# Kernel optimization log

Measured on AMD Instinct MI355X. Metric: run time of the kernel, lower is better.

Reference implementation:

```python
import jax, jax.numpy as jnp
import numpy as np

B = 32; H = 56; W = 56; C = 192; WS = 7; SHIFT = 3; NH = 6
HD = C // NH; N = WS * WS; MLP = 4 * C; NWH = H // WS; NWW = W // WS
EPS = 1e-5


def _rel_pos_index():
    coords = np.stack(np.meshgrid(np.arange(WS), np.arange(WS), indexing='ij'))  # (2,WS,WS)
    cf = coords.reshape(2, -1)                      # (2, N)
    rel = (cf[:, :, None] - cf[:, None, :]).transpose(1, 2, 0).astype(np.int64)  # (N,N,2)
    rel[..., 0] += WS - 1
    rel[..., 1] += WS - 1
    rel[..., 0] *= 2 * WS - 1
    return jnp.asarray(rel.sum(-1))                 # (N, N) int

REL_IDX = _rel_pos_index()


def _shift_mask():
    img = np.zeros((1, H, W, 1), np.float32)
    cnt = 0
    for hs in (slice(0, -WS), slice(-WS, -SHIFT), slice(-SHIFT, None)):
        for ws_ in (slice(0, -WS), slice(-WS, -SHIFT), slice(-SHIFT, None)):
            img[:, hs, ws_, :] = cnt
            cnt += 1
    mw = img.reshape(1, NWH, WS, NWW, WS, 1).transpose(0, 1, 3, 2, 4, 5).reshape(-1, N)
    am = mw[:, None, :] - mw[:, :, None]
    return jnp.asarray(np.where(am != 0, -100.0, 0.0).astype(np.float32))  # (nW, N, N)


def setup_inputs() -> dict:
    key = jax.random.key(0)
    ks = jax.random.split(key, 8)
    s = 0.02
    return {
        'x': jax.random.normal(ks[0], (B, H * W, C), jnp.float32),
        'attn_mask': _shift_mask(),
        'norm1_w': jnp.ones((C,), jnp.float32),
        'norm1_b': jnp.zeros((C,), jnp.float32),
        'qkv_w': jax.random.normal(ks[1], (3 * C, C), jnp.float32) * s,
        'qkv_b': jnp.zeros((3 * C,), jnp.float32),
        'rpb_table': jax.random.normal(ks[2], ((2 * WS - 1) ** 2, NH), jnp.float32) * s,
        'proj_w': jax.random.normal(ks[3], (C, C), jnp.float32) * s,
        'proj_b': jnp.zeros((C,), jnp.float32),
        'norm2_w': jnp.ones((C,), jnp.float32),
        'norm2_b': jnp.zeros((C,), jnp.float32),
        'fc1_w': jax.random.normal(ks[4], (MLP, C), jnp.float32) * s,
        'fc1_b': jnp.zeros((MLP,), jnp.float32),
        'fc2_w': jax.random.normal(ks[5], (C, MLP), jnp.float32) * s,
        'fc2_b': jnp.zeros((C,), jnp.float32),
    }


def _ln(x, w, b):
    m = jnp.mean(x, axis=-1, keepdims=True)
    v = jnp.mean(jnp.square(x - m), axis=-1, keepdims=True)
    return (x - m) * jax.lax.rsqrt(v + EPS) * w + b


def reference(x, attn_mask, norm1_w, norm1_b, qkv_w, qkv_b, rpb_table,
              proj_w, proj_b, norm2_w, norm2_b, fc1_w, fc1_b, fc2_w, fc2_b):
    shortcut = x
    xs = _ln(x, norm1_w, norm1_b).reshape(B, H, W, C)
    # cyclic shift
    xs = jnp.roll(xs, (-SHIFT, -SHIFT), axis=(1, 2))
    # window partition -> (B*nW, N, C)
    xw = xs.reshape(B, NWH, WS, NWW, WS, C).transpose(0, 1, 3, 2, 4, 5).reshape(-1, N, C)
    B_ = xw.shape[0]
    # qkv
    qkv = xw @ qkv_w.T + qkv_b                       # (B_, N, 3C)
    qkv = qkv.reshape(B_, N, 3, NH, HD).transpose(2, 0, 3, 1, 4)
    q, k, v = qkv[0], qkv[1], qkv[2]                 # (B_, NH, N, HD)
    scale = HD ** -0.5
    attn = jnp.einsum('bhnd,bhmd->bhnm', q * scale, k)
    # relative position bias: (N,N,NH) -> (NH,N,N)
    bias = rpb_table[REL_IDX.reshape(-1)].reshape(N, N, NH).transpose(2, 0, 1)
    attn = attn + bias[None]
    # shift mask: (nW, N, N)
    nW = attn_mask.shape[0]
    attn = attn.reshape(B_ // nW, nW, NH, N, N) + attn_mask[None, :, None]
    attn = jax.nn.softmax(attn.reshape(B_, NH, N, N), axis=-1)
    out = jnp.einsum('bhnm,bhmd->bhnd', attn, v)     # (B_, NH, N, HD)
    out = out.transpose(0, 2, 1, 3).reshape(B_, N, C)
    out = out @ proj_w.T + proj_b
    # window reverse -> (B, H, W, C)
    xr = out.reshape(B, NWH, NWW, WS, WS, C).transpose(0, 1, 3, 2, 4, 5).reshape(B, H, W, C)
    xr = jnp.roll(xr, (SHIFT, SHIFT), axis=(1, 2)).reshape(B, H * W, C)
    x = shortcut + xr
    # MLP
    h = _ln(x, norm2_w, norm2_b)
    h = jax.nn.gelu(h @ fc1_w.T + fc1_b, approximate=False)
    h = h @ fc2_w.T + fc2_b
    return x + h
```

## Files before the change

### kernel.cpp

```cpp
#include <hip/hip_runtime.h>
#include <hip/hip_bf16.h>

typedef unsigned short u16;
typedef __attribute__((ext_vector_type(8))) short bf16x8;
typedef __attribute__((ext_vector_type(4))) float f32x4;

#define MFMA16(a, b, c) __builtin_amdgcn_mfma_f32_16x16x32_bf16(a, b, c, 0, 0, 0)

__device__ __forceinline__ u16 f2b(float f) {
  union { float f; unsigned u; } x; x.f = f;
  return (u16)((x.u + 0x7fffu + ((x.u >> 16) & 1u)) >> 16);
}

__device__ __forceinline__ void gload_lds16(const void* g, void* l) {
  __builtin_amdgcn_global_load_lds(
      (const __attribute__((address_space(1))) void*)g,
      (__attribute__((address_space(3))) void*)l, 16, 0, 0);
}

template <int NCH>
__device__ __forceinline__ void stage_frags(const u16* __restrict__ src,
                                            u16* dst, int wave, int lane) {
#pragma unroll
  for (int it = 0; it < NCH / 4; ++it) {
    int chunk = it * 4 + wave;
    gload_lds16(src + ((size_t)chunk * 64 + lane) * 8, dst + chunk * 512);
  }
}

__device__ __forceinline__ void stage_64x192(const u16* __restrict__ src,
                                             int stride, u16* dst, int wave,
                                             int lane) {
#pragma unroll
  for (int it = 0; it < 6; ++it) {
    int id = (it * 4 + wave) * 64 + lane;
    int row = id / 24, ph = id - row * 24;
    int lch = (ph & 24) | ((ph ^ (row & 7)) & 7);
    gload_lds16(src + (size_t)row * stride + lch * 8,
                dst + (it * 4 + wave) * 512);
  }
}

__global__ __launch_bounds__(256) void pack_kernel(const float* __restrict__ W,
                                                   u16* __restrict__ F, int NT,
                                                   int KS, int K, int kmajor) {
  int f = blockIdx.x * 256 + threadIdx.x;
  if (f >= NT * KS * 64) return;
  int l = f & 63, rest = f >> 6;
  int ks, ct;
  if (kmajor) { ct = rest % NT; ks = rest / NT; }
  else        { ks = rest % KS; ct = rest / KS; }
  int row = ct * 16 + (l & 15);
  int col = ks * 32 + (l >> 4) * 8;
  const float* s = W + (size_t)row * K + col;
  u16* d = F + (size_t)f * 8;
#pragma unroll
  for (int i = 0; i < 8; ++i) d[i] = f2b(s[i]);
}

__global__ __launch_bounds__(256) void pack2_kernel(const float* __restrict__ W,
                                                    u16* __restrict__ F) {
  int f = blockIdx.x * 256 + threadIdx.x;
  if (f >= 24 * 12 * 64) return;
  int l = f & 63, rest = f >> 6;
  int ct = rest % 12, hs = rest / 12;
  int row = ct * 16 + (l & 15);
  int g = l >> 4;
  u16* d = F + (size_t)f * 8;
#pragma unroll
  for (int i = 0; i < 8; ++i) {
    int h = hs * 32 + (i < 4 ? 4 * g + i : 16 + 4 * g + (i - 4));
    d[i] = f2b(W[(size_t)row * 768 + h]);
  }
}

__global__ __launch_bounds__(256, 3) void attn_win(
    const float* __restrict__ x, const float* __restrict__ n1w,
    const float* __restrict__ n1b, const u16* __restrict__ qkvwf,
    const float* __restrict__ qkvb_, const float* __restrict__ rpb,
    const float* __restrict__ amask, u16* __restrict__ aout, int win0) {
  __shared__ __align__(16) u16 lds[25088];
  u16* wbuf = lds;
  u16* sA   = lds;
  u16* klds = lds + 18432;
  u16* vlds = lds + 21000;
  int tid = threadIdx.x, wave = tid >> 6, lane = tid & 63;
  int g = lane >> 4, c = lane & 15, wr = wave * 16;
  int blk = blockIdx.x;
  int wing = win0 + blk;
  int wi = wing & 63;
  {
    float vals[12][4];
    int srcrow[4];
#pragma unroll
    for (int reg = 0; reg < 4; ++reg) {
      int n = wr + 4 * g + reg;
      if (n > 48) n = 48;
      int bb = wing >> 6, wloc = wing & 63, wh = wloc >> 3, ww = wloc & 7;
      int rr = n / 7, cc = n - rr * 7;
      int hs = wh * 7 + rr + 3; if (hs >= 56) hs -= 56;
      int wsr = ww * 7 + cc + 3; if (wsr >= 56) wsr -= 56;
      srcrow[reg] = bb * 3136 + hs * 56 + wsr;
    }
#pragma unroll
    for (int nt = 0; nt < 12; ++nt)
#pragma unroll
      for (int reg = 0; reg < 4; ++reg)
        vals[nt][reg] = x[(size_t)srcrow[reg] * 192 + nt * 16 + c];
#pragma unroll
    for (int reg = 0; reg < 4; ++reg) {
      float s = 0.f;
#pragma unroll
      for (int nt = 0; nt < 12; ++nt) s += vals[nt][reg];
      s += __shfl_xor(s, 1, 64); s += __shfl_xor(s, 2, 64);
      s += __shfl_xor(s, 4, 64); s += __shfl_xor(s, 8, 64);
      float m = s * (1.f / 192.f), q = 0.f;
#pragma unroll
      for (int nt = 0; nt < 12; ++nt) { float d = vals[nt][reg] - m; q += d * d; }
      q += __shfl_xor(q, 1, 64); q += __shfl_xor(q, 2, 64);
      q += __shfl_xor(q, 4, 64); q += __shfl_xor(q, 8, 64);
      float rs = rsqrtf(q * (1.f / 192.f) + 1e-5f);
#pragma unroll
      for (int nt = 0; nt < 12; ++nt) vals[nt][reg] = (vals[nt][reg] - m) * rs;
    }
#pragma unroll
    for (int nt = 0; nt < 12; ++nt) {
      float wv = n1w[nt * 16 + c], bv = n1b[nt * 16 + c];
#pragma unroll
      for (int reg = 0; reg < 4; ++reg) {
        int r = wr + 4 * g + reg;
        int ch = nt * 2 + (c >> 3);
        int ph = (ch & 24) | ((ch ^ (r & 7)) & 7);
        sA[r * 192 + ph * 8 + (c & 7)] = f2b(vals[nt][reg] * wv + bv);
      }
    }
  }
  __syncthreads();
  bf16x8 afr[6];
  {
    int ar = wr + c;
#pragma unroll
    for (int ks = 0; ks < 6; ++ks) {
      int ch = ks * 4 + g;
      int ph = (ch & 24) | ((ch ^ (ar & 7)) & 7);
      afr[ks] = *(const bf16x8*)(sA + ar * 192 + ph * 8);
    }
  }
  __syncthreads();
#pragma unroll
  for (int s = 0; s < 3; ++s)
    stage_frags<12>(qkvwf + (size_t)((s * 12 + 0) * 6) * 512, wbuf + s * 6144,
                    wave, lane);
  int nq = wr + c;
  int nb = nq > 48 ? 48 : nq;
  int ridx[16];
  float pm[16];
  {
    int i1 = nb / 7, j1 = nb - i1 * 7;
#pragma unroll
    for (int kt = 0; kt < 4; ++kt)
#pragma unroll
      for (int reg = 0; reg < 4; ++reg) {
        int m = kt * 16 + 4 * g + reg;
        int idx = kt * 4 + reg;
        if (m < 49) {
          int i2 = m / 7, j2 = m - i2 * 7;
          ridx[idx] = ((i1 - i2 + 6) * 13 + (j1 - j2 + 6)) * 6;
          pm[idx] = amask[(size_t)wi * 2401 + nb * 49 + m];
        } else {
          ridx[idx] = 0;
          pm[idx] = -1e30f;
        }
      }
  }
  __syncthreads();
  for (int h = 0; h < 6; ++h) {
    f32x4 qa[2], ka[2], va[2];
#pragma unroll
    for (int s = 0; s < 3; ++s)
#pragma unroll
      for (int t = 0; t < 2; ++t) {
        f32x4 acc = {0.f, 0.f, 0.f, 0.f};
#pragma unroll
        for (int ks = 0; ks < 6; ++ks) {
          bf16x8 wf = *(const bf16x8*)(wbuf + (s * 12 + t * 6 + ks) * 512 +
                                       lane * 8);
          acc = MFMA16(wf, afr[ks], acc);
        }
        float4 b4 = *(const float4*)(qkvb_ + s * 192 + h * 32 + t * 16 + 4 * g);
#pragma unroll
        for (int reg = 0; reg < 4; ++reg) acc[reg] += ((const float*)&b4)[reg];
        if (s == 0) qa[t] = acc;
        else if (s == 1) ka[t] = acc;
        else va[t] = acc;
      }
    union { u16 hh[8]; bf16x8 v; } qf, kf;
#pragma unroll
    for (int reg = 0; reg < 4; ++reg) {
      qf.hh[reg] = f2b(qa[0][reg]);
      qf.hh[reg + 4] = f2b(qa[1][reg]);
      kf.hh[reg] = f2b(ka[0][reg]);
      kf.hh[reg + 4] = f2b(ka[1][reg]);
    }
    *(bf16x8*)(klds + nq * 40 + g * 8) = kf.v;
#pragma unroll
    for (int t = 0; t < 2; ++t)
#pragma unroll
      for (int reg = 0; reg < 4; ++reg)
        vlds[(t * 16 + 4 * g + reg) * 68 + nq] = f2b(va[t][reg]);
    __syncthreads();
    if (h < 5) {
#pragma unroll
      for (int s = 0; s < 3; ++s)
        stage_frags<12>(qkvwf + (size_t)((s * 12 + (h + 1) * 2) * 6) * 512,
                        wbuf + s * 6144, wave, lane);
    }
    float sv[16];
#pragma unroll
    for (int kt = 0; kt < 4; ++kt) {
      bf16x8 kw = *(const bf16x8*)(klds + (kt * 16 + c) * 40 + g * 8);
      f32x4 z = {0.f, 0.f, 0.f, 0.f};
      f32x4 sacc = MFMA16(kw, qf.v, z);
#pragma unroll
      for (int reg = 0; reg < 4; ++reg) sv[kt * 4 + reg] = sacc[reg];
    }
    const float scale = 0.17677669529663687f;
    float mx = -1e30f;
#pragma unroll
    for (int i = 0; i < 16; ++i) {
      sv[i] = sv[i] * scale + rpb[ridx[i] + h] + pm[i];
      mx = fmaxf(mx, sv[i]);
    }
    mx = fmaxf(mx, __shfl_xor(mx, 16, 64));
    mx = fmaxf(mx, __shfl_xor(mx, 32, 64));
    float se = 0.f;
#pragma unroll
    for (int i = 0; i < 16; ++i) {
      sv[i] = __expf(sv[i] - mx);
      se += sv[i];
    }
    se += __shfl_xor(se, 16, 64);
    se += __shfl_xor(se, 32, 64);
    float inv = 1.0f / se;
    union { u16 hh[8]; bf16x8 v; } pu0, pu1;
#pragma unroll
    for (int reg = 0; reg < 4; ++reg) {
      pu0.hh[reg] = f2b(sv[0 * 4 + reg] * inv);
      pu0.hh[reg + 4] = f2b(sv[1 * 4 + reg] * inv);
      pu1.hh[reg] = f2b(sv[2 * 4 + reg] * inv);
      pu1.hh[reg + 4] = f2b(sv[3 * 4 + reg] * inv);
    }
    f32x4 oacc[2] = {{0, 0, 0, 0}, {0, 0, 0, 0}};
#pragma unroll
    for (int nt = 0; nt < 2; ++nt)
#pragma unroll
      for (int mblk = 0; mblk < 2; ++mblk) {
        const u16* vp = vlds + (nt * 16 + c) * 68 + mblk * 32 + 4 * g;
        union { u16 hh[8]; bf16x8 v; } vt;
        *(short4*)(vt.hh) = *(const short4*)(vp);
        *(short4*)(vt.hh + 4) = *(const short4*)(vp + 16);
        oacc[nt] = MFMA16(vt.v, mblk ? pu1.v : pu0.v, oacc[nt]);
      }
    if (nq < 49) {
      u16* op = aout + ((size_t)blk * 49 + nq) * 192 + h * 32;
#pragma unroll
      for (int nt = 0; nt < 2; ++nt) {
        ushort4 st;
        st.x = f2b(oacc[nt][0]);
        st.y = f2b(oacc[nt][1]);
        st.z = f2b(oacc[nt][2]);
        st.w = f2b(oacc[nt][3]);
        *(ushort4*)(op + nt * 16 + 4 * g) = st;
      }
    }
    __syncthreads();
  }
}

__global__ __launch_bounds__(256, 3) void proj_fused(
    const u16* __restrict__ aout, const u16* __restrict__ wf,
    const float* __restrict__ pb, const float* __restrict__ x,
    float* __restrict__ out, int tok0) {
  __shared__ __align__(16) u16 lds[24576];
  u16* sA = lds;
  u16* b0 = lds;
  u16* b1 = lds + 12288;
  int tid = threadIdx.x, wave = tid >> 6, lane = tid & 63;
  int g = lane >> 4, c = lane & 15;
  int m0 = blockIdx.x * 64;
  stage_64x192(aout + (size_t)m0 * 192, 192, sA, wave, lane);
  asm volatile("s_waitcnt vmcnt(0)" ::: "memory");
  __syncthreads();
  int mw = wave >> 1, nw = wave & 1;
  bf16x8 afr[2][6];
#pragma unroll
  for (int rt = 0; rt < 2; ++rt) {
    int ar = mw * 32 + rt * 16 + c;
#pragma unroll
    for (int ks = 0; ks < 6; ++ks) {
      int ch = ks * 4 + g;
      int ph = (ch & 24) | ((ch ^ (ar & 7)) & 7);
      afr[rt][ks] = *(const bf16x8*)(sA + ar * 192 + ph * 8);
    }
  }
  size_t trow[2][4];
#pragma unroll
  for (int rt = 0; rt < 2; ++rt)
#pragma unroll
    for (int reg = 0; reg < 4; ++reg) {
      int rg = tok0 + m0 + mw * 32 + rt * 16 + 4 * g + reg;
      int win = rg / 49, n = rg - win * 49;
      int b_ = win >> 6, wi = win & 63;
      int wh = wi >> 3, ww = wi & 7;
      int rr = n / 7, cc = n - rr * 7;
      int hd_ = wh * 7 + rr + 3; if (hd_ >= 56) hd_ -= 56;
      int wd = ww * 7 + cc + 3; if (wd >= 56) wd -= 56;
      trow[rt][reg] = (size_t)b_ * 3136 + hd_ * 56 + wd;
    }
  __syncthreads();
  stage_frags<24>(wf, b0, wave, lane);
  __syncthreads();
  for (int j = 0; j < 3; ++j) {
    const u16* cb = (j & 1) ? b1 : b0;
    if (j < 2)
      stage_frags<24>(wf + (size_t)(j + 1) * 24 * 512, (j & 1) ? b0 : b1, wave,
                      lane);
    f32x4 S[2][2] = {{{0,0,0,0},{0,0,0,0}},{{0,0,0,0},{0,0,0,0}}};
#pragma unroll
    for (int nt = 0; nt < 2; ++nt)
#pragma unroll
      for (int ks = 0; ks < 6; ++ks) {
        bf16x8 bf = *(const bf16x8*)(cb + ((nw * 2 + nt) * 6 + ks) * 512 + lane * 8);
        S[0][nt] = MFMA16(afr[0][ks], bf, S[0][nt]);
        S[1][nt] = MFMA16(afr[1][ks], bf, S[1][nt]);
      }
#pragma unroll
    for (int nt = 0; nt < 2; ++nt) {
      int jc = j * 64 + nw * 32 + nt * 16 + c;
      float bv = pb[jc];
#pragma unroll
      for (int rt = 0; rt < 2; ++rt)
#pragma unroll
        for (int reg = 0; reg < 4; ++reg) {
          size_t o = trow[rt][reg] * 192 + jc;
          out[o] = x[o] + S[rt][nt][reg] + bv;
        }
    }
    __syncthreads();
  }
}

__global__ __launch_bounds__(256, 3) void mlp_fused(
    const float* __restrict__ n2w, const float* __restrict__ n2b,
    const u16* __restrict__ w1f, const float* __restrict__ b1,
    const u16* __restrict__ w2f, const float* __restrict__ b2,
    float* __restrict__ out) {
  __shared__ __align__(16) u16 lds[24576];
  u16* c1a = lds;
  u16* c1b = lds + 6144;
  u16* c2a = lds + 12288;
  u16* c2b = lds + 18432;
  u16* sA  = lds;
  int tid = threadIdx.x, wave = tid >> 6, lane = tid & 63;
  int g = lane >> 4, c = lane & 15, wr = wave * 16;
  int m0 = blockIdx.x * 64;
  {
    float v[12][4];
    int rr[4];
#pragma unroll
    for (int reg = 0; reg < 4; ++reg) rr[reg] = m0 + wr + 4 * g + reg;
#pragma unroll
    for (int nt = 0; nt < 12; ++nt)
#pragma unroll
      for (int reg = 0; reg < 4; ++reg)
        v[nt][reg] = out[(size_t)rr[reg] * 192 + nt * 16 + c];
#pragma unroll
    for (int reg = 0; reg < 4; ++reg) {
      float s = 0.f;
#pragma unroll
      for (int nt = 0; nt < 12; ++nt) s += v[nt][reg];
      s += __shfl_xor(s, 1, 64); s += __shfl_xor(s, 2, 64);
      s += __shfl_xor(s, 4, 64); s += __shfl_xor(s, 8, 64);
      float m = s * (1.f / 192.f), q = 0.f;
#pragma unroll
      for (int nt = 0; nt < 12; ++nt) { float d = v[nt][reg] - m; q += d * d; }
      q += __shfl_xor(q, 1, 64); q += __shfl_xor(q, 2, 64);
      q += __shfl_xor(q, 4, 64); q += __shfl_xor(q, 8, 64);
      float rs = rsqrtf(q * (1.f / 192.f) + 1e-5f);
#pragma unroll
      for (int nt = 0; nt < 12; ++nt) v[nt][reg] = (v[nt][reg] - m) * rs;
    }
#pragma unroll
    for (int nt = 0; nt < 12; ++nt) {
      float wv = n2w[nt * 16 + c], bv = n2b[nt * 16 + c];
#pragma unroll
      for (int reg = 0; reg < 4; ++reg) {
        int r = wr + 4 * g + reg;
        int ch = nt * 2 + (c >> 3);
        int ph = (ch & 24) | ((ch ^ (r & 7)) & 7);
        sA[r * 192 + ph * 8 + (c & 7)] = f2b(v[nt][reg] * wv + bv);
      }
    }
  }
  __syncthreads();
  bf16x8 afr[6];
  {
    int ar = wr + c;
#pragma unroll
    for (int ks = 0; ks < 6; ++ks) {
      int ch = ks * 4 + g;
      int ph = (ch & 24) | ((ch ^ (ar & 7)) & 7);
      afr[ks] = *(const bf16x8*)(sA + ar * 192 + ph * 8);
    }
  }
  __syncthreads();
  stage_frags<12>(w1f, c1a, wave, lane);
  stage_frags<12>(w2f, c2a, wave, lane);
  f32x4 o[12];
#pragma unroll
  for (int i = 0; i < 12; ++i) o[i] = (f32x4){0.f, 0.f, 0.f, 0.f};
  __syncthreads();
  for (int j = 0; j < 24; ++j) {
    int cur = j & 1;
    const u16* r1 = cur ? c1b : c1a;
    const u16* r2 = cur ? c2b : c2a;
    if (j < 23) {
      stage_frags<12>(w1f + (size_t)(j + 1) * 6144, cur ? c1a : c1b, wave, lane);
      stage_frags<12>(w2f + (size_t)(j + 1) * 6144, cur ? c2a : c2b, wave, lane);
    }
    f32x4 S1[2] = {{0,0,0,0},{0,0,0,0}};
#pragma unroll
    for (int ks = 0; ks < 6; ++ks) {
      bf16x8 w0 = *(const bf16x8*)(r1 + (0 * 6 + ks) * 512 + lane * 8);
      bf16x8 w1v = *(const bf16x8*)(r1 + (1 * 6 + ks) * 512 + lane * 8);
      S1[0] = MFMA16(w0, afr[ks], S1[0]);
      S1[1] = MFMA16(w1v, afr[ks], S1[1]);
    }
    union { u16 h[8]; bf16x8 v; } pu;
    float4 bv0 = *(const float4*)(b1 + j * 32 + 4 * g);
    float4 bv1 = *(const float4*)(b1 + j * 32 + 16 + 4 * g);
#pragma unroll
    for (int r = 0; r < 4; ++r) {
      float v0 = S1[0][r] + ((const float*)&bv0)[r];
      float u20 = v0 * (1.5957691216f + 0.0713548163f * v0 * v0);
      pu.h[r] = f2b(v0 / (1.f + __expf(-u20)));
      float v1 = S1[1][r] + ((const float*)&bv1)[r];
      float u21 = v1 * (1.5957691216f + 0.0713548163f * v1 * v1);
      pu.h[r + 4] = f2b(v1 / (1.f + __expf(-u21)));
    }
#pragma unroll
    for (int ct = 0; ct < 12; ++ct) {
      bf16x8 wf2 = *(const bf16x8*)(r2 + ct * 512 + lane * 8);
      o[ct] = MFMA16(wf2, pu.v, o[ct]);
    }
    __syncthreads();
  }
  size_t rowoff = (size_t)(m0 + wr + c) * 192;
#pragma unroll
  for (int ct = 0; ct < 12; ++ct) {
    float4 b4 = *(const float4*)(b2 + ct * 16 + 4 * g);
#pragma unroll
    for (int r = 0; r < 4; ++r) {
      size_t oo = rowoff + ct * 16 + 4 * g + r;
      out[oo] = out[oo] + o[ct][r] + ((const float*)&b4)[r];
    }
  }
}

extern "C" void kernel_launch(void* const* d_in, const int* in_sizes, int n_in,
                              void* d_out, int out_size, void* d_ws, size_t ws_size,
                              hipStream_t stream) {
  (void)in_sizes; (void)n_in; (void)out_size;
  const float* x     = (const float*)d_in[0];
  const float* amask = (const float*)d_in[1];
  const float* n1w   = (const float*)d_in[2];
  const float* n1b   = (const float*)d_in[3];
  const float* qkvw  = (const float*)d_in[4];
  const float* qkvb  = (const float*)d_in[5];
  const float* rpb   = (const float*)d_in[6];
  const float* projw = (const float*)d_in[7];
  const float* projb = (const float*)d_in[8];
  const float* n2w   = (const float*)d_in[9];
  const float* n2b   = (const float*)d_in[10];
  const float* fc1w  = (const float*)d_in[11];
  const float* fc1b  = (const float*)d_in[12];
  const float* fc2w  = (const float*)d_in[13];
  const float* fc2b  = (const float*)d_in[14];
  float* out = (float*)d_out;
  char* ws = (char*)d_ws;

  u16* qkvwf = (u16*)(ws);
  u16* projwf = (u16*)(ws + 221184);
  u16* fc1wf = (u16*)(ws + 221184 + 73728);
  u16* fc2wf = (u16*)(ws + 221184 + 73728 + 294912);
  char* arena = ws + (1 << 20);
  size_t arena_sz = ws_size > (1 << 20) ? ws_size - (1 << 20) : 0;

  pack_kernel<<<(36 * 6 * 64 + 255) / 256, 256, 0, stream>>>(qkvw, qkvwf, 36, 6, 192, 0);
  pack_kernel<<<(12 * 6 * 64 + 255) / 256, 256, 0, stream>>>(projw, projwf, 12, 6, 192, 0);
  pack_kernel<<<(48 * 6 * 64 + 255) / 256, 256, 0, stream>>>(fc1w, fc1wf, 48, 6, 192, 0);
  pack2_kernel<<<(24 * 12 * 64 + 255) / 256, 256, 0, stream>>>(fc2w, fc2wf);

  int NCA = 1;
  while (NCA < 16 && (size_t)(2048 / NCA) * 49 * 192 * 2 > arena_sz) NCA <<= 1;
  int Wc = 2048 / NCA;
  for (int cch = 0; cch < NCA; ++cch) {
    int win0 = cch * Wc;
    int tok0 = win0 * 49;
    u16* aout_c = (u16*)arena;
    int rows = Wc * 49;
    attn_win<<<Wc, 256, 0, stream>>>(x, n1w, n1b, qkvwf, qkvb, rpb, amask,
                                     aout_c, win0);
    proj_fused<<<rows / 64, 256, 0, stream>>>(aout_c, projwf, projb, x, out,
                                              tok0);
  }

  mlp_fused<<<1568, 256, 0, stream>>>(n2w, n2b, fc1wf, fc1b, fc2wf, fc2b,
                                      out);
}
```

Baseline: 265.9 us.

## Enlarge MLP block to 128 rows with 8 waves sharing staged weights

The fused MLP kernel now runs 512 threads per block and covers 128 rows instead of 64. Each double-buffered fc1/fc2 weight fragment staged into LDS is therefore reused by twice as many rows, which cuts weight load traffic and staging work per row. Staging is spread over 8 waves with a new helper, and the residual epilogue now uses float4 read-modify-write instead of scalar accesses. In exchange, LDS use and register pressure per block rise, and the grid drops to 784 blocks, which changes wave-quantization and occupancy.

```diff
diff --git a/kernel.cpp b/kernel.cpp
--- a/kernel.cpp
+++ b/kernel.cpp
@@ -25,6 +25,21 @@
   for (int it = 0; it < NCH / 4; ++it) {
     int chunk = it * 4 + wave;
     gload_lds16(src + ((size_t)chunk * 64 + lane) * 8, dst + chunk * 512);
+  }
+}
+
+__device__ __forceinline__ void stage12x2_512(const u16* __restrict__ s1,
+                                              u16* d1,
+                                              const u16* __restrict__ s2,
+                                              u16* d2, int wave, int lane) {
+#pragma unroll
+  for (int it = 0; it < 3; ++it) {
+    int id = it * 8 + wave;
+    if (id < 12)
+      gload_lds16(s1 + ((size_t)id * 64 + lane) * 8, d1 + id * 512);
+    else
+      gload_lds16(s2 + ((size_t)(id - 12) * 64 + lane) * 8,
+                  d2 + (id - 12) * 512);
   }
 }
 
@@ -350,7 +365,7 @@
   }
 }
 
-__global__ __launch_bounds__(256, 3) void mlp_fused(
+__global__ __launch_bounds__(512, 2) void mlp_fused(
     const float* __restrict__ n2w, const float* __restrict__ n2b,
     const u16* __restrict__ w1f, const float* __restrict__ b1,
     const u16* __restrict__ w2f, const float* __restrict__ b2,
@@ -363,7 +378,7 @@
   u16* sA  = lds;
   int tid = threadIdx.x, wave = tid >> 6, lane = tid & 63;
   int g = lane >> 4, c = lane & 15, wr = wave * 16;
-  int m0 = blockIdx.x * 64;
+  int m0 = blockIdx.x * 128;
   {
     float v[12][4];
     int rr[4];
@@ -414,8 +429,7 @@
     }
   }
   __syncthreads();
-  stage_frags<12>(w1f, c1a, wave, lane);
-  stage_frags<12>(w2f, c2a, wave, lane);
+  stage12x2_512(w1f, c1a, w2f, c2a, wave, lane);
   f32x4 o[12];
 #pragma unroll
   for (int i = 0; i < 12; ++i) o[i] = (f32x4){0.f, 0.f, 0.f, 0.f};
@@ -424,10 +438,9 @@
     int cur = j & 1;
     const u16* r1 = cur ? c1b : c1a;
     const u16* r2 = cur ? c2b : c2a;
-    if (j < 23) {
-      stage_frags<12>(w1f + (size_t)(j + 1) * 6144, cur ? c1a : c1b, wave, lane);
-      stage_frags<12>(w2f + (size_t)(j + 1) * 6144, cur ? c2a : c2b, wave, lane);
-    }
+    if (j < 23)
+      stage12x2_512(w1f + (size_t)(j + 1) * 6144, cur ? c1a : c1b,
+                    w2f + (size_t)(j + 1) * 6144, cur ? c2a : c2b, wave, lane);
     f32x4 S1[2] = {{0,0,0,0},{0,0,0,0}};
 #pragma unroll
     for (int ks = 0; ks < 6; ++ks) {
@@ -455,15 +468,17 @@
     }
     __syncthreads();
   }
-  size_t rowoff = (size_t)(m0 + wr + c) * 192;
+  float* rowp = out + (size_t)(m0 + wr + c) * 192;
 #pragma unroll
   for (int ct = 0; ct < 12; ++ct) {
+    float4* p = (float4*)(rowp + ct * 16 + 4 * g);
+    float4 cu = *p;
     float4 b4 = *(const float4*)(b2 + ct * 16 + 4 * g);
-#pragma unroll
-    for (int r = 0; r < 4; ++r) {
-      size_t oo = rowoff + ct * 16 + 4 * g + r;
-      out[oo] = out[oo] + o[ct][r] + ((const float*)&b4)[r];
-    }
+    cu.x += o[ct][0] + b4.x;
+    cu.y += o[ct][1] + b4.y;
+    cu.z += o[ct][2] + b4.z;
+    cu.w += o[ct][3] + b4.w;
+    *p = cu;
   }
 }
 
@@ -515,6 +530,6 @@
                                               tok0);
   }
 
-  mlp_fused<<<1568, 256, 0, stream>>>(n2w, n2b, fc1wf, fc1b, fc2wf, fc2b,
-                                      out);
-}
+  mlp_fused<<<784, 512, 0, stream>>>(n2w, n2b, fc1wf, fc1b, fc2wf, fc2b,
+                                     out);
+}
```

New measurement: 285.2 us. 1.07x slower.

## Fuse output projection and residual into attention window kernel

Applied to the files above, without the earlier changes.

The separate proj kernel and its bf16 attention-output buffer are removed. Each attention block keeps per-head outputs in registers as MFMA B-fragments, then stages a repacked projection weight (two halves) into LDS and computes proj plus bias plus residual directly, writing to the un-shifted token rows. This removes a global write and read of the attention output and a kernel launch, at the cost of more registers and per-block weight staging in attn_win.

```diff
diff --git a/kernel.cpp b/kernel.cpp
--- a/kernel.cpp
+++ b/kernel.cpp
@@ -25,19 +25,6 @@
   for (int it = 0; it < NCH / 4; ++it) {
     int chunk = it * 4 + wave;
     gload_lds16(src + ((size_t)chunk * 64 + lane) * 8, dst + chunk * 512);
-  }
-}
-
-__device__ __forceinline__ void stage_64x192(const u16* __restrict__ src,
-                                             int stride, u16* dst, int wave,
-                                             int lane) {
-#pragma unroll
-  for (int it = 0; it < 6; ++it) {
-    int id = (it * 4 + wave) * 64 + lane;
-    int row = id / 24, ph = id - row * 24;
-    int lch = (ph & 24) | ((ph ^ (row & 7)) & 7);
-    gload_lds16(src + (size_t)row * stride + lch * 8,
-                dst + (it * 4 + wave) * 512);
   }
 }
 
@@ -74,11 +61,29 @@
   }
 }
 
+__global__ __launch_bounds__(256) void pack_proj_pi(const float* __restrict__ W,
+                                                    u16* __restrict__ F) {
+  int f = blockIdx.x * 256 + threadIdx.x;
+  if (f >= 72 * 64) return;
+  int l = f & 63, rest = f >> 6;
+  int half = rest / 36, r2 = rest - half * 36;
+  int ks = r2 / 6, ctl = r2 - ks * 6;
+  int row = (half * 6 + ctl) * 16 + (l & 15);
+  int g = l >> 4;
+  u16* d = F + (size_t)f * 8;
+#pragma unroll
+  for (int i = 0; i < 8; ++i) {
+    int k = ks * 32 + (i < 4 ? 4 * g + i : 16 + 4 * g + (i - 4));
+    d[i] = f2b(W[(size_t)row * 192 + k]);
+  }
+}
+
 __global__ __launch_bounds__(256, 3) void attn_win(
     const float* __restrict__ x, const float* __restrict__ n1w,
     const float* __restrict__ n1b, const u16* __restrict__ qkvwf,
     const float* __restrict__ qkvb_, const float* __restrict__ rpb,
-    const float* __restrict__ amask, u16* __restrict__ aout, int win0) {
+    const float* __restrict__ amask, const u16* __restrict__ pwf,
+    const float* __restrict__ pb, float* __restrict__ out) {
   __shared__ __align__(16) u16 lds[25088];
   u16* wbuf = lds;
   u16* sA   = lds;
@@ -86,8 +91,7 @@
   u16* vlds = lds + 21000;
   int tid = threadIdx.x, wave = tid >> 6, lane = tid & 63;
   int g = lane >> 4, c = lane & 15, wr = wave * 16;
-  int blk = blockIdx.x;
-  int wing = win0 + blk;
+  int wing = blockIdx.x;
   int wi = wing & 63;
   {
     float vals[12][4];
@@ -174,6 +178,8 @@
       }
   }
   __syncthreads();
+  bf16x8 ofr[6];
+#pragma unroll
   for (int h = 0; h < 6; ++h) {
     f32x4 qa[2], ka[2], va[2];
 #pragma unroll
@@ -261,90 +267,60 @@
         *(short4*)(vt.hh + 4) = *(const short4*)(vp + 16);
         oacc[nt] = MFMA16(vt.v, mblk ? pu1.v : pu0.v, oacc[nt]);
       }
+    {
+      union { u16 hh[8]; bf16x8 v; } of_;
+#pragma unroll
+      for (int reg = 0; reg < 4; ++reg) {
+        of_.hh[reg] = f2b(oacc[0][reg]);
+        of_.hh[reg + 4] = f2b(oacc[1][reg]);
+      }
+      ofr[h] = of_.v;
+    }
+    __syncthreads();
+  }
+  size_t trow = 0;
+  if (nq < 49) {
+    int rr = nq / 7, cc2 = nq - rr * 7;
+    int wloc = wing & 63, wh = wloc >> 3, ww2 = wloc & 7;
+    int hs2 = wh * 7 + rr + 3; if (hs2 >= 56) hs2 -= 56;
+    int ws2 = ww2 * 7 + cc2 + 3; if (ws2 >= 56) ws2 -= 56;
+    trow = (size_t)(wing >> 6) * 3136 + hs2 * 56 + ws2;
+  }
+#pragma unroll
+  for (int half = 0; half < 2; ++half) {
+#pragma unroll
+    for (int it = 0; it < 9; ++it) {
+      int chunk = it * 4 + wave;
+      gload_lds16(pwf + ((size_t)(half * 36 + chunk) * 64 + lane) * 8,
+                  lds + chunk * 512);
+    }
+    asm volatile("s_waitcnt vmcnt(0)" ::: "memory");
+    __syncthreads();
+    f32x4 op6[6];
+#pragma unroll
+    for (int i = 0; i < 6; ++i) op6[i] = (f32x4){0.f, 0.f, 0.f, 0.f};
+#pragma unroll
+    for (int ks = 0; ks < 6; ++ks)
+#pragma unroll
+      for (int ctl = 0; ctl < 6; ++ctl) {
+        bf16x8 wf = *(const bf16x8*)(lds + (ks * 6 + ctl) * 512 + lane * 8);
+        op6[ctl] = MFMA16(wf, ofr[ks], op6[ctl]);
+      }
     if (nq < 49) {
-      u16* op = aout + ((size_t)blk * 49 + nq) * 192 + h * 32;
-#pragma unroll
-      for (int nt = 0; nt < 2; ++nt) {
-        ushort4 st;
-        st.x = f2b(oacc[nt][0]);
-        st.y = f2b(oacc[nt][1]);
-        st.z = f2b(oacc[nt][2]);
-        st.w = f2b(oacc[nt][3]);
-        *(ushort4*)(op + nt * 16 + 4 * g) = st;
-      }
-    }
-    __syncthreads();
-  }
-}
-
-__global__ __launch_bounds__(256, 3) void proj_fused(
-    const u16* __restrict__ aout, const u16* __restrict__ wf,
-    const float* __restrict__ pb, const float* __restrict__ x,
-    float* __restrict__ out, int tok0) {
-  __shared__ __align__(16) u16 lds[24576];
-  u16* sA = lds;
-  u16* b0 = lds;
-  u16* b1 = lds + 12288;
-  int tid = threadIdx.x, wave = tid >> 6, lane = tid & 63;
-  int g = lane >> 4, c = lane & 15;
-  int m0 = blockIdx.x * 64;
-  stage_64x192(aout + (size_t)m0 * 192, 192, sA, wave, lane);
-  asm volatile("s_waitcnt vmcnt(0)" ::: "memory");
-  __syncthreads();
-  int mw = wave >> 1, nw = wave & 1;
-  bf16x8 afr[2][6];
-#pragma unroll
-  for (int rt = 0; rt < 2; ++rt) {
-    int ar = mw * 32 + rt * 16 + c;
-#pragma unroll
-    for (int ks = 0; ks < 6; ++ks) {
-      int ch = ks * 4 + g;
-      int ph = (ch & 24) | ((ch ^ (ar & 7)) & 7);
-      afr[rt][ks] = *(const bf16x8*)(sA + ar * 192 + ph * 8);
-    }
-  }
-  size_t trow[2][4];
-#pragma unroll
-  for (int rt = 0; rt < 2; ++rt)
-#pragma unroll
-    for (int reg = 0; reg < 4; ++reg) {
-      int rg = tok0 + m0 + mw * 32 + rt * 16 + 4 * g + reg;
-      int win = rg / 49, n = rg - win * 49;
-      int b_ = win >> 6, wi = win & 63;
-      int wh = wi >> 3, ww = wi & 7;
-      int rr = n / 7, cc = n - rr * 7;
-      int hd_ = wh * 7 + rr + 3; if (hd_ >= 56) hd_ -= 56;
-      int wd = ww * 7 + cc + 3; if (wd >= 56) wd -= 56;
-      trow[rt][reg] = (size_t)b_ * 3136 + hd_ * 56 + wd;
-    }
-  __syncthreads();
-  stage_frags<24>(wf, b0, wave, lane);
-  __syncthreads();
-  for (int j = 0; j < 3; ++j) {
-    const u16* cb = (j & 1) ? b1 : b0;
-    if (j < 2)
-      stage_frags<24>(wf + (size_t)(j + 1) * 24 * 512, (j & 1) ? b0 : b1, wave,
-                      lane);
-    f32x4 S[2][2] = {{{0,0,0,0},{0,0,0,0}},{{0,0,0,0},{0,0,0,0}}};
-#pragma unroll
-    for (int nt = 0; nt < 2; ++nt)
-#pragma unroll
-      for (int ks = 0; ks < 6; ++ks) {
-        bf16x8 bf = *(const bf16x8*)(cb + ((nw * 2 + nt) * 6 + ks) * 512 + lane * 8);
-        S[0][nt] = MFMA16(afr[0][ks], bf, S[0][nt]);
-        S[1][nt] = MFMA16(afr[1][ks], bf, S[1][nt]);
-      }
-#pragma unroll
-    for (int nt = 0; nt < 2; ++nt) {
-      int jc = j * 64 + nw * 32 + nt * 16 + c;
-      float bv = pb[jc];
-#pragma unroll
-      for (int rt = 0; rt < 2; ++rt)
-#pragma unroll
-        for (int reg = 0; reg < 4; ++reg) {
-          size_t o = trow[rt][reg] * 192 + jc;
-          out[o] = x[o] + S[rt][nt][reg] + bv;
-        }
+      float* rowp = out + trow * 192 + half * 96;
+      const float* xp = x + trow * 192 + half * 96;
+#pragma unroll
+      for (int ctl = 0; ctl < 6; ++ctl) {
+        int colo = ctl * 16 + 4 * g;
+        float4 xv = *(const float4*)(xp + colo);
+        float4 b4 = *(const float4*)(pb + half * 96 + colo);
+        float4 st;
+        st.x = xv.x + op6[ctl][0] + b4.x;
+        st.y = xv.y + op6[ctl][1] + b4.y;
+        st.z = xv.z + op6[ctl][2] + b4.z;
+        st.w = xv.w + op6[ctl][3] + b4.w;
+        *(float4*)(rowp + colo) = st;
+      }
     }
     __syncthreads();
   }
@@ -470,7 +446,7 @@
 extern "C" void kernel_launch(void* const* d_in, const int* in_sizes, int n_in,
                               void* d_out, int out_size, void* d_ws, size_t ws_size,
                               hipStream_t stream) {
-  (void)in_sizes; (void)n_in; (void)out_size;
+  (void)in_sizes; (void)n_in; (void)out_size; (void)ws_size;
   const float* x     = (const float*)d_in[0];
   const float* amask = (const float*)d_in[1];
   const float* n1w   = (const float*)d_in[2];
@@ -493,27 +469,14 @@
   u16* projwf = (u16*)(ws + 221184);
   u16* fc1wf = (u16*)(ws + 221184 + 73728);
   u16* fc2wf = (u16*)(ws + 221184 + 73728 + 294912);
-  char* arena = ws + (1 << 20);
-  size_t arena_sz = ws_size > (1 << 20) ? ws_size - (1 << 20) : 0;
 
   pack_kernel<<<(36 * 6 * 64 + 255) / 256, 256, 0, stream>>>(qkvw, qkvwf, 36, 6, 192, 0);
-  pack_kernel<<<(12 * 6 * 64 + 255) / 256, 256, 0, stream>>>(projw, projwf, 12, 6, 192, 0);
+  pack_proj_pi<<<(72 * 64 + 255) / 256, 256, 0, stream>>>(projw, projwf);
   pack_kernel<<<(48 * 6 * 64 + 255) / 256, 256, 0, stream>>>(fc1w, fc1wf, 48, 6, 192, 0);
   pack2_kernel<<<(24 * 12 * 64 + 255) / 256, 256, 0, stream>>>(fc2w, fc2wf);
 
-  int NCA = 1;
-  while (NCA < 16 && (size_t)(2048 / NCA) * 49 * 192 * 2 > arena_sz) NCA <<= 1;
-  int Wc = 2048 / NCA;
-  for (int cch = 0; cch < NCA; ++cch) {
-    int win0 = cch * Wc;
-    int tok0 = win0 * 49;
-    u16* aout_c = (u16*)arena;
-    int rows = Wc * 49;
-    attn_win<<<Wc, 256, 0, stream>>>(x, n1w, n1b, qkvwf, qkvb, rpb, amask,
-                                     aout_c, win0);
-    proj_fused<<<rows / 64, 256, 0, stream>>>(aout_c, projwf, projb, x, out,
-                                              tok0);
-  }
+  attn_win<<<2048, 256, 0, stream>>>(x, n1w, n1b, qkvwf, qkvb, rpb, amask,
+                                     projwf, projb, out);
 
   mlp_fused<<<1568, 256, 0, stream>>>(n2w, n2b, fc1wf, fc1b, fc2wf, fc2b,
                                       out);
```

Result: faster. 254.5 us (-4.3%).
